# Optimization experiments

Hardware: AMD Instinct MI355X
Metric: run time of the kernel (lower is better)

The kernel has to match this reference:

```python
import jax, jax.numpy as jnp
import numpy as np

HIDDEN = 768
HEADS = 12
HEAD_DIM = HIDDEN // HEADS  # 64


def setup_inputs() -> dict:
    key = jax.random.key(0)
    ks = jax.random.split(key, 7)
    B, S = 4, 2048
    std = 0.02
    return {
        "hidden_states": jax.random.normal(ks[0], (B, S, HIDDEN), dtype=jnp.float32),
        "attention_mask": jnp.zeros((B, 1, 1, S), dtype=jnp.float32),
        "Wq": jax.random.normal(ks[1], (HIDDEN, HIDDEN), dtype=jnp.float32) * std,
        "bq": jnp.zeros((HIDDEN,), dtype=jnp.float32),
        "Wk": jax.random.normal(ks[2], (HIDDEN, HIDDEN), dtype=jnp.float32) * std,
        "bk": jnp.zeros((HIDDEN,), dtype=jnp.float32),
        "Wv": jax.random.normal(ks[3], (HIDDEN, HIDDEN), dtype=jnp.float32) * std,
        "bv": jnp.zeros((HIDDEN,), dtype=jnp.float32),
    }


def _split_heads(x):
    # [B, S, HIDDEN] -> [B, H, S, D]
    B, S, _ = x.shape
    return x.reshape(B, S, HEADS, HEAD_DIM).transpose(0, 2, 1, 3)


def reference(hidden_states, attention_mask, Wq, bq, Wk, bk, Wv, bv):
    q = _split_heads(hidden_states @ Wq + bq)
    k = _split_heads(hidden_states @ Wk + bk)
    v = _split_heads(hidden_states @ Wv + bv)
    # [B, H, S, S] full score matrix (as in the original non-fused impl)
    scores = jnp.einsum("bhqd,bhkd->bhqk", q, k) / jnp.sqrt(
        jnp.asarray(HEAD_DIM, dtype=q.dtype)
    )
    scores = scores + attention_mask
    probs = jax.nn.softmax(scores, axis=-1)
    # dropout prob = 0.0 -> identity in eval
    ctx = jnp.einsum("bhqk,bhkd->bhqd", probs, v)
    B, H, S, D = ctx.shape
    return ctx.transpose(0, 2, 1, 3).reshape(B, S, H * D)
```

## Files before the change

### kernel.cpp

```cpp
#include <hip/hip_runtime.h>

typedef __bf16 bf16;
typedef __attribute__((ext_vector_type(8))) __bf16 bf16x8;
typedef __attribute__((ext_vector_type(4))) __bf16 bf16x4;
typedef __attribute__((ext_vector_type(4))) float f32x4;
typedef __attribute__((ext_vector_type(16))) float f32x16;
typedef __attribute__((ext_vector_type(4))) unsigned int u32x4;

#define DI __device__ __forceinline__

static constexpr int HID = 768;
static constexpr int SEQ = 2048;
static constexpr int NH  = 12;
static constexpr int HD  = 64;

DI void gload16(const void* g, void* l) {
  __builtin_amdgcn_global_load_lds(
      (const __attribute__((address_space(1))) void*)g,
      (__attribute__((address_space(3))) void*)l, 16, 0, 0);
}
DI int swz128(int row, int cb) { return row * 128 + (cb ^ ((row & 7) << 4)); }

DI unsigned cvtpk_bf16(float lo, float hi) {
  unsigned d;
  asm("v_cvt_pk_bf16_f32 %0, %1, %2" : "=v"(d) : "v"(lo), "v"(hi));
  return d;
}
DI void permswap(unsigned &a, unsigned &b) {
  asm("v_permlane32_swap_b32 %0, %1" : "+v"(a), "+v"(b));
}

__global__ void k_pre(const float* __restrict__ X, bf16* __restrict__ Xb, int n8,
                      const float* __restrict__ Wq, const float* __restrict__ Wk,
                      const float* __restrict__ Wv, bf16* __restrict__ WT) {
  __shared__ float t[64][65];
  int bx = blockIdx.x;
  if (bx < 3072) {
    int i = bx * blockDim.x + threadIdx.x;
    if (i >= n8) return;
    const f32x4* Xv = (const f32x4*)X;
    f32x4 a = Xv[2 * i], b = Xv[2 * i + 1];
    bf16x8 o;
    o[0] = (bf16)a[0]; o[1] = (bf16)a[1]; o[2] = (bf16)a[2]; o[3] = (bf16)a[3];
    o[4] = (bf16)b[0]; o[5] = (bf16)b[1]; o[6] = (bf16)b[2]; o[7] = (bf16)b[3];
    *(bf16x8*)(Xb + (size_t)i * 8) = o;
    return;
  }
  int tt2 = bx - 3072;
  int z = tt2 / 144;
  int rem = tt2 - z * 144;
  int ny = rem / 12, kx = rem % 12;
  const float* W = (z == 0) ? Wq : (z == 1) ? Wk : Wv;
  bf16* WTz = WT + (size_t)z * HID * HID;
  int k0 = kx * 64, n0 = ny * 64;
  int tt = threadIdx.x;
  for (int p = 0; p < 4; ++p) {
    int r = p * 16 + (tt >> 4), c4 = (tt & 15) * 4;
    f32x4 v = *(const f32x4*)(W + (size_t)(k0 + r) * HID + n0 + c4);
    t[c4 + 0][r] = v[0]; t[c4 + 1][r] = v[1]; t[c4 + 2][r] = v[2]; t[c4 + 3][r] = v[3];
  }
  __syncthreads();
  for (int p = 0; p < 4; ++p) {
    int rn = p * 16 + (tt >> 4), c4 = (tt & 15) * 4;
    bf16x4 o;
    o[0] = (bf16)t[rn][c4]; o[1] = (bf16)t[rn][c4 + 1];
    o[2] = (bf16)t[rn][c4 + 2]; o[3] = (bf16)t[rn][c4 + 3];
    *(bf16x4*)(WTz + (size_t)(n0 + rn) * HID + k0 + c4) = o;
  }
}

__global__ __launch_bounds__(256, 2)
void k_qkv_gemm(const bf16* __restrict__ Xb, const bf16* __restrict__ WT,
                const float* __restrict__ bq, const float* __restrict__ bk,
                const float* __restrict__ bv,
                bf16* __restrict__ Qb, bf16* __restrict__ Kb, bf16* __restrict__ VTb) {
  int z = blockIdx.z;
  const bf16* WTz = WT + (size_t)z * HID * HID;
  const float* bias = (z == 0) ? bq : (z == 1) ? bk : bv;

  int m0 = blockIdx.x * 128, n0 = blockIdx.y * 128;
  __shared__ char lds[32768];
  int w = threadIdx.x >> 6, l = threadIdx.x & 63;
  int wr = w >> 1, wc = w & 1;

  f32x4 acc[4][4] = {};

  for (int it = 0; it < HID / 64; ++it) {
    int k0 = it * 64;
    __syncthreads();
    for (int j = 0; j < 8; ++j) {
      int base = w * 8192 + j * 1024;
      int o = base + l * 16;
      const char* src;
      if (o < 16384) {
        int row = o >> 7;
        int cb = (o & 127) ^ ((row & 7) << 4);
        src = (const char*)(Xb + (size_t)(m0 + row) * HID + k0) + cb;
      } else {
        int o2 = o - 16384;
        int row = o2 >> 7;
        int cb = (o2 & 127) ^ ((row & 7) << 4);
        src = (const char*)(WTz + (size_t)(n0 + row) * HID + k0) + cb;
      }
      gload16(src, lds + base);
    }
    __syncthreads();

    for (int kk = 0; kk < 2; ++kk) {
      bf16x8 af[4], bfr[4];
      int cb = kk * 64 + ((l >> 4) << 4);
      for (int ms = 0; ms < 4; ++ms) {
        int row = wr * 64 + ms * 16 + (l & 15);
        af[ms] = *(const bf16x8*)(lds + swz128(row, cb));
      }
      for (int ns = 0; ns < 4; ++ns) {
        int row = wc * 64 + ns * 16 + (l & 15);
        bfr[ns] = *(const bf16x8*)(lds + 16384 + swz128(row, cb));
      }
      for (int ms = 0; ms < 4; ++ms)
        for (int ns = 0; ns < 4; ++ns)
          acc[ms][ns] = __builtin_amdgcn_mfma_f32_16x16x32_bf16(af[ms], bfr[ns], acc[ms][ns], 0, 0, 0);
    }
  }

  if (z == 2) {
    #pragma unroll
    for (int ns = 0; ns < 4; ++ns) {
      int col = n0 + wc * 64 + ns * 16 + (l & 15);
      float bvv = bias[col];
      int h = col >> 6, d = col & 63;
      #pragma unroll
      for (int ms = 0; ms < 4; ++ms) {
        int m = m0 + wr * 64 + ms * 16 + ((l >> 4) << 2);
        int bb = m >> 11, s = m & 2047;
        bf16x4 pk;
        #pragma unroll
        for (int r = 0; r < 4; ++r) pk[r] = (bf16)(acc[ms][ns][r] + bvv);
        size_t base = (size_t)(bb * NH + h) * HD * SEQ;
        size_t idx = base + (size_t)(s >> 6) * 4096 + (size_t)((s >> 3) & 7) * 512
                     + (size_t)d * 8 + (s & 7);
        *(bf16x4*)(VTb + idx) = pk;
      }
    }
  } else if (z == 1) {
    for (int ns = 0; ns < 4; ++ns) {
      int col = n0 + wc * 64 + ns * 16 + (l & 15);
      float bvv = bias[col];
      int h = col >> 6, d = col & 63;
      for (int ms = 0; ms < 4; ++ms) {
        for (int r = 0; r < 4; ++r) {
          int m = m0 + wr * 64 + ms * 16 + ((l >> 4) << 2) + r;
          int bb = m >> 11, s = m & 2047;
          float v = acc[ms][ns][r] + bvv;
          size_t base = (size_t)(bb * NH + h) * SEQ * HD;
          size_t idx = base + (size_t)(s >> 6) * 4096 + (size_t)(d >> 3) * 512
                       + (size_t)(s & 63) * 8 + (d & 7);
          Kb[idx] = (bf16)v;
        }
      }
    }
  } else {
    for (int ns = 0; ns < 4; ++ns) {
      int col = n0 + wc * 64 + ns * 16 + (l & 15);
      float bvv = bias[col];
      int h = col >> 6, d = col & 63;
      for (int ms = 0; ms < 4; ++ms) {
        for (int r = 0; r < 4; ++r) {
          int m = m0 + wr * 64 + ms * 16 + ((l >> 4) << 2) + r;
          int bb = m >> 11, s = m & 2047;
          float v = (acc[ms][ns][r] + bvv) * 0.125f;
          Qb[(((size_t)(bb * NH + h) * SEQ + s) << 6) + d] = (bf16)v;
        }
      }
    }
  }
}

__global__ __launch_bounds__(256, 4)
void k_attn(const bf16* __restrict__ Qb, const bf16* __restrict__ Kb,
            const bf16* __restrict__ VTb, const float* __restrict__ mask,
            float* __restrict__ out) {
  __shared__ char lds[33280];
  constexpr int NT = SEQ / 64;
  int bh = blockIdx.x;
  int b = bh / NH, h = bh % NH;
  int q0 = blockIdx.y * 128;
  int w = threadIdx.x >> 6, l = threadIdx.x & 63;
  int q = l & 31, hi = l >> 5;
  const bf16* Qp = Qb + (size_t)bh * SEQ * HD;
  const char* Kbase = (const char*)(Kb + (size_t)bh * SEQ * HD);
  const char* VTbase = (const char*)(VTb + (size_t)bh * HD * SEQ);
  const float* mb = mask + (size_t)b * SEQ;

  bf16x8 qf[4];
  #pragma unroll
  for (int dstep = 0; dstep < 4; ++dstep)
    qf[dstep] = *(const bf16x8*)(Qp + (size_t)(q0 + w * 32 + q) * HD + dstep * 16 + hi * 8);

  f32x16 acc[2] = {};
  float psum = 0.f;

  int rbase = hi * 1024 + q * 16;

  auto stage = [&](int c, int kt) {
    size_t t = (size_t)kt * 8192;
    int off = w * 2048;
    #pragma unroll
    for (int j = 0; j < 2; ++j)
      gload16(Kbase + t + off + j * 1024 + l * 16,
              lds + c * 16384 + off + j * 1024);
    #pragma unroll
    for (int j = 0; j < 2; ++j)
      gload16(VTbase + t + off + j * 1024 + l * 16,
              lds + c * 16384 + 8192 + off + j * 1024);
  };

  stage(0, 0);
  __syncthreads();

  int cur = 0;
  for (int kt = 0; kt < NT; ++kt) {
    if (kt + 1 < NT) stage(cur ^ 1, kt + 1);

    f32x4 mm[2][4];
    #pragma unroll
    for (int kh = 0; kh < 2; ++kh)
      #pragma unroll
      for (int blk = 0; blk < 4; ++blk)
        mm[kh][blk] = *(const f32x4*)(mb + kt * 64 + kh * 32 + blk * 8 + hi * 4);

    const char* Kl = lds + cur * 16384 + rbase;
    const char* Vl = lds + cur * 16384 + 8192 + rbase;

    #pragma unroll
    for (int kh = 0; kh < 2; ++kh) {
      bf16x8 kfh[4], vfk[4];
      #pragma unroll
      for (int dstep = 0; dstep < 4; ++dstep)
        kfh[dstep] = *(const bf16x8*)(Kl + dstep * 2048 + kh * 512);
      #pragma unroll
      for (int half = 0; half < 2; ++half)
        #pragma unroll
        for (int db = 0; db < 2; ++db)
          vfk[half * 2 + db] =
              *(const bf16x8*)(Vl + (kh * 2 + half) * 2048 + db * 512);

      f32x16 p;
      #pragma unroll
      for (int r = 0; r < 16; ++r) p[r] = mm[kh][r >> 2][r & 3];
      __builtin_amdgcn_s_setprio(1);
      #pragma unroll
      for (int dstep = 0; dstep < 4; ++dstep)
        p = __builtin_amdgcn_mfma_f32_32x32x16_bf16(kfh[dstep], qf[dstep], p, 0, 0, 0);
      __builtin_amdgcn_s_setprio(0);

      #pragma unroll
      for (int r = 0; r < 16; ++r) {
        float e = __expf(p[r]);
        p[r] = e;
        psum += e;
      }

      #pragma unroll
      for (int half = 0; half < 2; ++half) {
        int base = half * 8;
        unsigned a0 = cvtpk_bf16(p[base + 0], p[base + 1]);
        unsigned a1 = cvtpk_bf16(p[base + 2], p[base + 3]);
        unsigned a2 = cvtpk_bf16(p[base + 4], p[base + 5]);
        unsigned a3 = cvtpk_bf16(p[base + 6], p[base + 7]);
        permswap(a0, a2);
        permswap(a1, a3);
        u32x4 pk; pk[0] = a0; pk[1] = a1; pk[2] = a2; pk[3] = a3;
        bf16x8 PA = __builtin_bit_cast(bf16x8, pk);
        __builtin_amdgcn_s_setprio(1);
        #pragma unroll
        for (int db = 0; db < 2; ++db)
          acc[db] = __builtin_amdgcn_mfma_f32_32x32x16_bf16(PA, vfk[half * 2 + db], acc[db], 0, 0, 0);
        __builtin_amdgcn_s_setprio(0);
      }
    }

    __syncthreads();
    cur ^= 1;
  }

  float tot = psum + __shfl_xor(psum, 32);
  float* lsumL = (float*)(lds + 32768 + w * 128);
  if (l < 32) lsumL[l] = tot;
  __syncthreads();
  f32x4 lv[4];
  #pragma unroll
  for (int blk = 0; blk < 4; ++blk)
    lv[blk] = *(const f32x4*)(lsumL + blk * 8 + hi * 4);
  float inv[16];
  #pragma unroll
  for (int r = 0; r < 16; ++r) inv[r] = 1.0f / lv[r >> 2][r & 3];

  #pragma unroll
  for (int db = 0; db < 2; ++db)
    #pragma unroll
    for (int r = 0; r < 16; ++r) {
      int s = q0 + w * 32 + (r & 3) + 8 * (r >> 2) + 4 * hi;
      out[((size_t)(b * SEQ + s)) * HID + h * HD + db * 32 + q] = acc[db][r] * inv[r];
    }
}

extern "C" void kernel_launch(void* const* d_in, const int* in_sizes, int n_in,
                              void* d_out, int out_size, void* d_ws, size_t ws_size,
                              hipStream_t stream) {
  const float* X    = (const float*)d_in[0];
  const float* mask = (const float*)d_in[1];
  const float* Wq   = (const float*)d_in[2];
  const float* bq   = (const float*)d_in[3];
  const float* Wk   = (const float*)d_in[4];
  const float* bk   = (const float*)d_in[5];
  const float* Wv   = (const float*)d_in[6];
  const float* bv   = (const float*)d_in[7];
  float* out = (float*)d_out;
  char* ws = (char*)d_ws;

  const size_t SZ_XB = (size_t)8192 * HID * 2;
  const size_t SZ_WT = (size_t)3 * HID * HID * 2;
  const size_t SZ_M  = (size_t)4 * NH * SEQ * HD * 2;
  bf16* Xb  = (bf16*)(ws);
  bf16* WT  = (bf16*)(ws + SZ_XB);
  bf16* Qb  = (bf16*)(ws + SZ_XB + SZ_WT);
  bf16* Kb  = (bf16*)(ws + SZ_XB + SZ_WT + SZ_M);
  bf16* VTb = (bf16*)(ws + SZ_XB + SZ_WT + 2 * SZ_M);

  k_pre<<<3504, 256, 0, stream>>>(X, Xb, 8192 * HID / 8, Wq, Wk, Wv, WT);
  k_qkv_gemm<<<dim3(64, 6, 3), 256, 0, stream>>>(Xb, WT, bq, bk, bv, Qb, Kb, VTb);
  k_attn<<<dim3(48, 16), 256, 0, stream>>>(Qb, Kb, VTb, mask, out);
}
```

Baseline: 119.4 us.

## Split attention key tiles across wave pairs with LDS reduction of partial outputs

Doubles the attention block to 512 threads so each pair of waves shares one 32-query group, with each wave handling one 32-key half of every 64-key tile. The partial P·V accumulators and row sums from the second wave are reduced through LDS at the end, and the first wave of each pair writes the normalized output. This raises the number of waves in flight to hide MFMA and exp latency and spreads the per-tile staging loads over more threads. In exchange it adds an end-of-kernel LDS reduction and extra barriers, and each wave does half the work per barrier.

```diff
diff --git a/kernel.cpp b/kernel.cpp
--- a/kernel.cpp
+++ b/kernel.cpp
@@ -176,26 +176,28 @@
   }
 }
 
-__global__ __launch_bounds__(256, 4)
+__global__ __launch_bounds__(512, 6)
 void k_attn(const bf16* __restrict__ Qb, const bf16* __restrict__ Kb,
             const bf16* __restrict__ VTb, const float* __restrict__ mask,
             float* __restrict__ out) {
-  __shared__ char lds[33280];
+  __shared__ char lds[34048];
   constexpr int NT = SEQ / 64;
   int bh = blockIdx.x;
   int b = bh / NH, h = bh % NH;
   int q0 = blockIdx.y * 128;
   int w = threadIdx.x >> 6, l = threadIdx.x & 63;
+  int g = w >> 1, kh = w & 1;
   int q = l & 31, hi = l >> 5;
   const bf16* Qp = Qb + (size_t)bh * SEQ * HD;
   const char* Kbase = (const char*)(Kb + (size_t)bh * SEQ * HD);
   const char* VTbase = (const char*)(VTb + (size_t)bh * HD * SEQ);
   const float* mb = mask + (size_t)b * SEQ;
 
+  int sq = q0 + g * 32 + q;
   bf16x8 qf[4];
   #pragma unroll
   for (int dstep = 0; dstep < 4; ++dstep)
-    qf[dstep] = *(const bf16x8*)(Qp + (size_t)(q0 + w * 32 + q) * HD + dstep * 16 + hi * 8);
+    qf[dstep] = *(const bf16x8*)(Qp + (size_t)sq * HD + dstep * 16 + hi * 8);
 
   f32x16 acc[2] = {};
   float psum = 0.f;
@@ -204,15 +206,9 @@
 
   auto stage = [&](int c, int kt) {
     size_t t = (size_t)kt * 8192;
-    int off = w * 2048;
-    #pragma unroll
-    for (int j = 0; j < 2; ++j)
-      gload16(Kbase + t + off + j * 1024 + l * 16,
-              lds + c * 16384 + off + j * 1024);
-    #pragma unroll
-    for (int j = 0; j < 2; ++j)
-      gload16(VTbase + t + off + j * 1024 + l * 16,
-              lds + c * 16384 + 8192 + off + j * 1024);
+    int off = w * 1024;
+    gload16(Kbase + t + off + l * 16, lds + c * 16384 + off);
+    gload16(VTbase + t + off + l * 16, lds + c * 16384 + 8192 + off);
   };
 
   stage(0, 0);
@@ -222,87 +218,95 @@
   for (int kt = 0; kt < NT; ++kt) {
     if (kt + 1 < NT) stage(cur ^ 1, kt + 1);
 
-    f32x4 mm[2][4];
-    #pragma unroll
-    for (int kh = 0; kh < 2; ++kh)
-      #pragma unroll
-      for (int blk = 0; blk < 4; ++blk)
-        mm[kh][blk] = *(const f32x4*)(mb + kt * 64 + kh * 32 + blk * 8 + hi * 4);
+    f32x4 mm[4];
+    #pragma unroll
+    for (int blk = 0; blk < 4; ++blk)
+      mm[blk] = *(const f32x4*)(mb + kt * 64 + kh * 32 + blk * 8 + hi * 4);
 
     const char* Kl = lds + cur * 16384 + rbase;
     const char* Vl = lds + cur * 16384 + 8192 + rbase;
 
-    #pragma unroll
-    for (int kh = 0; kh < 2; ++kh) {
-      bf16x8 kfh[4], vfk[4];
+    bf16x8 kfh[4];
+    #pragma unroll
+    for (int dstep = 0; dstep < 4; ++dstep)
+      kfh[dstep] = *(const bf16x8*)(Kl + dstep * 2048 + kh * 512);
+
+    f32x16 p;
+    #pragma unroll
+    for (int r = 0; r < 16; ++r) p[r] = mm[r >> 2][r & 3];
+    __builtin_amdgcn_s_setprio(1);
+    #pragma unroll
+    for (int dstep = 0; dstep < 4; ++dstep)
+      p = __builtin_amdgcn_mfma_f32_32x32x16_bf16(kfh[dstep], qf[dstep], p, 0, 0, 0);
+    __builtin_amdgcn_s_setprio(0);
+
+    #pragma unroll
+    for (int r = 0; r < 16; ++r) {
+      float e = __expf(p[r]);
+      p[r] = e;
+      psum += e;
+    }
+
+    #pragma unroll
+    for (int half = 0; half < 2; ++half) {
+      bf16x8 vfa = *(const bf16x8*)(Vl + (kh * 2 + half) * 2048 + 0 * 512);
+      bf16x8 vfb = *(const bf16x8*)(Vl + (kh * 2 + half) * 2048 + 1 * 512);
+      int base = half * 8;
+      unsigned a0 = cvtpk_bf16(p[base + 0], p[base + 1]);
+      unsigned a1 = cvtpk_bf16(p[base + 2], p[base + 3]);
+      unsigned a2 = cvtpk_bf16(p[base + 4], p[base + 5]);
+      unsigned a3 = cvtpk_bf16(p[base + 6], p[base + 7]);
+      permswap(a0, a2);
+      permswap(a1, a3);
+      u32x4 pk; pk[0] = a0; pk[1] = a1; pk[2] = a2; pk[3] = a3;
+      bf16x8 PA = __builtin_bit_cast(bf16x8, pk);
+      __builtin_amdgcn_s_setprio(1);
+      acc[0] = __builtin_amdgcn_mfma_f32_32x32x16_bf16(PA, vfa, acc[0], 0, 0, 0);
+      acc[1] = __builtin_amdgcn_mfma_f32_32x32x16_bf16(PA, vfb, acc[1], 0, 0, 0);
+      __builtin_amdgcn_s_setprio(0);
+    }
+
+    __syncthreads();
+    cur ^= 1;
+  }
+
+  float tot = psum + __shfl_xor(psum, 32);
+  float* ldsf = (float*)lds;
+  if (kh == 1) {
+    #pragma unroll
+    for (int db = 0; db < 2; ++db)
       #pragma unroll
-      for (int dstep = 0; dstep < 4; ++dstep)
-        kfh[dstep] = *(const bf16x8*)(Kl + dstep * 2048 + kh * 512);
+      for (int r = 0; r < 16; ++r)
+        ldsf[g * 2048 + db * 1024 + r * 64 + l] = acc[db][r];
+    if (l < 32) ldsf[8192 + g * 32 + l] = tot;
+  }
+  __syncthreads();
+  if (kh == 0) {
+    #pragma unroll
+    for (int db = 0; db < 2; ++db)
       #pragma unroll
-      for (int half = 0; half < 2; ++half)
-        #pragma unroll
-        for (int db = 0; db < 2; ++db)
-          vfk[half * 2 + db] =
-              *(const bf16x8*)(Vl + (kh * 2 + half) * 2048 + db * 512);
-
-      f32x16 p;
-      #pragma unroll
-      for (int r = 0; r < 16; ++r) p[r] = mm[kh][r >> 2][r & 3];
-      __builtin_amdgcn_s_setprio(1);
-      #pragma unroll
-      for (int dstep = 0; dstep < 4; ++dstep)
-        p = __builtin_amdgcn_mfma_f32_32x32x16_bf16(kfh[dstep], qf[dstep], p, 0, 0, 0);
-      __builtin_amdgcn_s_setprio(0);
-
+      for (int r = 0; r < 16; ++r)
+        acc[db][r] += ldsf[g * 2048 + db * 1024 + r * 64 + l];
+    if (l < 32) ldsf[8192 + 128 + g * 32 + l] = tot + ldsf[8192 + g * 32 + l];
+  }
+  __syncthreads();
+  if (kh == 0) {
+    f32x4 lv[4];
+    #pragma unroll
+    for (int blk = 0; blk < 4; ++blk)
+      lv[blk] = *(const f32x4*)(ldsf + 8192 + 128 + g * 32 + blk * 8 + hi * 4);
+    float inv[16];
+    #pragma unroll
+    for (int r = 0; r < 16; ++r) inv[r] = 1.0f / lv[r >> 2][r & 3];
+
+    #pragma unroll
+    for (int db = 0; db < 2; ++db)
       #pragma unroll
       for (int r = 0; r < 16; ++r) {
-        float e = __expf(p[r]);
-        p[r] = e;
-        psum += e;
-      }
-
-      #pragma unroll
-      for (int half = 0; half < 2; ++half) {
-        int base = half * 8;
-        unsigned a0 = cvtpk_bf16(p[base + 0], p[base + 1]);
-        unsigned a1 = cvtpk_bf16(p[base + 2], p[base + 3]);
-        unsigned a2 = cvtpk_bf16(p[base + 4], p[base + 5]);
-        unsigned a3 = cvtpk_bf16(p[base + 6], p[base + 7]);
-        permswap(a0, a2);
-        permswap(a1, a3);
-        u32x4 pk; pk[0] = a0; pk[1] = a1; pk[2] = a2; pk[3] = a3;
-        bf16x8 PA = __builtin_bit_cast(bf16x8, pk);
-        __builtin_amdgcn_s_setprio(1);
-        #pragma unroll
-        for (int db = 0; db < 2; ++db)
-          acc[db] = __builtin_amdgcn_mfma_f32_32x32x16_bf16(PA, vfk[half * 2 + db], acc[db], 0, 0, 0);
-        __builtin_amdgcn_s_setprio(0);
-      }
-    }
-
-    __syncthreads();
-    cur ^= 1;
-  }
-
-  float tot = psum + __shfl_xor(psum, 32);
-  float* lsumL = (float*)(lds + 32768 + w * 128);
-  if (l < 32) lsumL[l] = tot;
-  __syncthreads();
-  f32x4 lv[4];
-  #pragma unroll
-  for (int blk = 0; blk < 4; ++blk)
-    lv[blk] = *(const f32x4*)(lsumL + blk * 8 + hi * 4);
-  float inv[16];
-  #pragma unroll
-  for (int r = 0; r < 16; ++r) inv[r] = 1.0f / lv[r >> 2][r & 3];
-
-  #pragma unroll
-  for (int db = 0; db < 2; ++db)
-    #pragma unroll
-    for (int r = 0; r < 16; ++r) {
-      int s = q0 + w * 32 + (r & 3) + 8 * (r >> 2) + 4 * hi;
-      out[((size_t)(b * SEQ + s)) * HID + h * HD + db * 32 + q] = acc[db][r] * inv[r];
-    }
+        int s = q0 + g * 32 + (r & 3) + 8 * (r >> 2) + 4 * hi;
+        out[((size_t)(b * SEQ + s)) * HID + h * HD + db * 32 + q] = acc[db][r] * inv[r];
+      }
+  }
 }
 
 extern "C" void kernel_launch(void* const* d_in, const int* in_sizes, int n_in,
@@ -330,5 +334,5 @@
 
   k_pre<<<3504, 256, 0, stream>>>(X, Xb, 8192 * HID / 8, Wq, Wk, Wv, WT);
   k_qkv_gemm<<<dim3(64, 6, 3), 256, 0, stream>>>(Xb, WT, bq, bk, bv, Qb, Kb, VTb);
-  k_attn<<<dim3(48, 16), 256, 0, stream>>>(Qb, Kb, VTb, mask, out);
-}
+  k_attn<<<dim3(48, 16), 512, 0, stream>>>(Qb, Kb, VTb, mask, out);
+}
```

Result: slower. 166.7 us (+39.6%).
